# Kernel tuning notes

Measured on AMD Instinct MI355X. Metric: run time of the kernel, lower is better.

The kernel has to match this reference:

```python
import jax, jax.numpy as jnp
import numpy as np

DIM = 96
DIM_OUT = 192
HEADS = 2
Q_STRIDE = 4
WINDOW_SIZE = 16  # flattened mask-unit size AFTER q pooling
HEAD_DIM = DIM_OUT // HEADS


def setup_inputs() -> dict:
    key = jax.random.key(0)
    k1, k2, k3, k4, k5 = jax.random.split(key, 5)
    B, N = 64, 3136  # 56x56 tokens, 49 windows of 64 tokens
    x = jax.random.normal(k1, (B, N, DIM), dtype=jnp.float32)
    # nn.Linear params (PyTorch layout: [out, in])
    s_qkv = 1.0 / np.sqrt(DIM)
    w_qkv = jax.random.uniform(k2, (3 * DIM_OUT, DIM), jnp.float32, -s_qkv, s_qkv)
    b_qkv = jax.random.uniform(k3, (3 * DIM_OUT,), jnp.float32, -s_qkv, s_qkv)
    s_proj = 1.0 / np.sqrt(DIM_OUT)
    w_proj = jax.random.uniform(k4, (DIM_OUT, DIM_OUT), jnp.float32, -s_proj, s_proj)
    b_proj = jax.random.uniform(k5, (DIM_OUT,), jnp.float32, -s_proj, s_proj)
    return {"x": x, "w_qkv": w_qkv, "b_qkv": b_qkv, "w_proj": w_proj, "b_proj": b_proj}


def reference(x, w_qkv, b_qkv, w_proj, b_proj):
    B, N, _ = x.shape
    num_windows = N // (Q_STRIDE * WINDOW_SIZE)
    tokens_per_win = Q_STRIDE * WINDOW_SIZE  # 64
    # QKV projection; token axis splits as (tokens_per_win, num_windows)
    qkv = (x @ w_qkv.T + b_qkv).reshape(B, tokens_per_win, num_windows, 3, HEADS, HEAD_DIM)
    qkv = jnp.transpose(qkv, (3, 0, 4, 2, 1, 5))  # [3, B, H, W, T, D]
    q, k, v = qkv[0], qkv[1], qkv[2]
    # q pooling via strided amax over q_stride
    q = q.reshape(B, HEADS, num_windows, Q_STRIDE, WINDOW_SIZE, HEAD_DIM).max(axis=3)
    scale = HEAD_DIM ** (-0.5)
    attn = jax.nn.softmax(jnp.einsum('bhwqd,bhwkd->bhwqk', q * scale, k), axis=-1)
    o = jnp.einsum('bhwqk,bhwkd->bhwqd', attn, v)  # [B, H, W, WINDOW_SIZE, D]
    # transpose(1,3) then flatten -> [B, WINDOW_SIZE*num_windows, dim_out]
    o = jnp.transpose(o, (0, 3, 2, 1, 4)).reshape(B, -1, DIM_OUT)
    return o @ w_proj.T + b_proj
```

## Files before the change

### kernel.cpp

```cpp
#include <hip/hip_runtime.h>


#define NW 49
#define NTOK 3136
#define DIM 96
#define DOUT 192

#define WSQ 0
#define WSBQ 55296
#define WSP 55872
#define WSBP 92736
#define WSTOT 92928

typedef __bf16 bf16x8 __attribute__((ext_vector_type(8)));
typedef float f32x4 __attribute__((ext_vector_type(4)));
typedef unsigned short u16x8 __attribute__((ext_vector_type(8)));
typedef unsigned short u16x4 __attribute__((ext_vector_type(4)));

__device__ __forceinline__ unsigned short f2bf(float f) {
    unsigned int u = __builtin_bit_cast(unsigned int, f);
    u = (u + 0x7FFFu + ((u >> 16) & 1u)) >> 16;
    return (unsigned short)u;
}
__device__ __forceinline__ float bf2f(unsigned short h) {
    unsigned int u = ((unsigned int)h) << 16;
    return __builtin_bit_cast(float, u);
}

__device__ __forceinline__ bool sniff_fp32(const unsigned short* x16) {
    int sane = 0;
    #pragma unroll
    for (int i = 0; i < 32; ++i) {
        unsigned e = ((unsigned)x16[2 * i] >> 7) & 0xFFu;
        sane += (e >= 100u && e <= 141u) ? 1 : 0;
    }
    return sane < 24;
}

__device__ __forceinline__ bf16x8 ldb(const unsigned short* p) {
    return __builtin_bit_cast(bf16x8, *(const u16x8*)p);
}

__global__ __launch_bounds__(256)
void conv_weights(const void* __restrict__ x,
                  const void* __restrict__ w_qkv, const void* __restrict__ b_qkv,
                  const void* __restrict__ w_proj, const void* __restrict__ b_proj,
                  unsigned short* __restrict__ ws)
{
    const bool f32m = sniff_fp32((const unsigned short*)x);
    int t = blockIdx.x * 256 + threadIdx.x;
    if (t >= WSTOT / 8) return;
    int off = t * 8;
    const void* src;
    int rel;
    if (off < WSBQ)      { src = w_qkv;  rel = off; }
    else if (off < WSP)  { src = b_qkv;  rel = off - WSBQ; }
    else if (off < WSBP) { src = w_proj; rel = off - WSP; }
    else                 { src = b_proj; rel = off - WSBP; }
    u16x8 v;
    if (f32m) {
        const float* p = (const float*)src + rel;
        f32x4 a = *(const f32x4*)p;
        f32x4 bb = *(const f32x4*)(p + 4);
        v[0] = f2bf(a[0]);  v[1] = f2bf(a[1]);  v[2] = f2bf(a[2]);  v[3] = f2bf(a[3]);
        v[4] = f2bf(bb[0]); v[5] = f2bf(bb[1]); v[6] = f2bf(bb[2]); v[7] = f2bf(bb[3]);
    } else {
        v = *(const u16x8*)((const unsigned short*)src + rel);
    }
    *(u16x8*)(ws + off) = v;
}

__global__ __launch_bounds__(256, 2)
void mua_main(const void* __restrict__ x,
              const unsigned short* __restrict__ ws,
              void* __restrict__ out)
{
    const int bid = blockIdx.x;
    const int b   = bid / NW;
    const int wi  = bid - b * NW;
    const int tid  = threadIdx.x;
    const int wave = tid >> 6;
    const int lane = tid & 63;
    const int quad = lane >> 4;
    const int l16  = lane & 15;

    __shared__ __attribute__((aligned(16))) unsigned short lds[32768];
    unsigned short* k_s  = lds;
    unsigned short* v_s  = lds + 13312;
    unsigned short* qp_s = lds + 27136;
    unsigned short* p_s  = lds + 30464;
    unsigned short* x_s  = k_s;
    unsigned short* o_s  = qp_s;

    const int nbase = wave * 144;
    bf16x8 wfr[9][3];
    float  biasq[9];
    #pragma unroll
    for (int nt = 0; nt < 9; ++nt) {
        const int c = nbase + nt * 16 + l16;
        #pragma unroll
        for (int ks = 0; ks < 3; ++ks)
            wfr[nt][ks] = ldb(ws + WSQ + c * 96 + ks * 32 + quad * 8);
        biasq[nt] = bf2f(ws[WSBQ + c]);
    }

    const bool f32m = sniff_fp32((const unsigned short*)x);

    {
        const size_t xoff = ((size_t)b * NTOK + wi) * DIM;
        if (f32m) {
            #pragma unroll
            for (int i = 0; i < 3; ++i) {
                int chunk = tid + i * 256;
                int row = chunk / 12;
                int c16 = chunk - row * 12;
                const float* p = (const float*)x + xoff + (size_t)row * (NW * DIM) + c16 * 8;
                f32x4 a = *(const f32x4*)p;
                f32x4 bb = *(const f32x4*)(p + 4);
                u16x8 r;
                r[0] = f2bf(a[0]);  r[1] = f2bf(a[1]);  r[2] = f2bf(a[2]);  r[3] = f2bf(a[3]);
                r[4] = f2bf(bb[0]); r[5] = f2bf(bb[1]); r[6] = f2bf(bb[2]); r[7] = f2bf(bb[3]);
                *(u16x8*)&x_s[row * 104 + c16 * 8] = r;
            }
        } else {
            #pragma unroll
            for (int i = 0; i < 3; ++i) {
                int chunk = tid + i * 256;
                int row = chunk / 12;
                int c16 = chunk - row * 12;
                const unsigned short* p = (const unsigned short*)x + xoff + (size_t)row * (NW * DIM) + c16 * 8;
                *(u16x8*)&x_s[row * 104 + c16 * 8] = *(const u16x8*)p;
            }
        }
    }
    __syncthreads();

    bf16x8 afr[4][3];
    #pragma unroll
    for (int mt = 0; mt < 4; ++mt)
        #pragma unroll
        for (int ks = 0; ks < 3; ++ks)
            afr[mt][ks] = ldb(&x_s[(mt * 16 + l16) * 104 + ks * 32 + quad * 8]);
    __syncthreads();

    #pragma unroll
    for (int nt = 0; nt < 9; ++nt) {
        f32x4 acc[4];
        #pragma unroll
        for (int mt = 0; mt < 4; ++mt) {
            acc[mt] = (f32x4){0.f, 0.f, 0.f, 0.f};
            #pragma unroll
            for (int ks = 0; ks < 3; ++ks)
                acc[mt] = __builtin_amdgcn_mfma_f32_16x16x32_bf16(afr[mt][ks], wfr[nt][ks], acc[mt], 0, 0, 0);
        }
        const int c = nbase + nt * 16 + l16;
        const float bias = biasq[nt];
        const int type = c / 192;
        const int hd   = (c % 192) / 96;
        const int d    = c % 96;
        if (type == 0) {
            #pragma unroll
            for (int r = 0; r < 4; ++r) {
                float m = fmaxf(fmaxf(acc[0][r], acc[1][r]), fmaxf(acc[2][r], acc[3][r])) + bias;
                qp_s[(hd * 16 + quad * 4 + r) * 104 + d] = f2bf(m);
            }
        } else if (type == 1) {
            #pragma unroll
            for (int mt = 0; mt < 4; ++mt)
                #pragma unroll
                for (int r = 0; r < 4; ++r)
                    k_s[hd * 6656 + (mt * 16 + quad * 4 + r) * 104 + d] = f2bf(acc[mt][r] + bias);
        } else {
            #pragma unroll
            for (int mt = 0; mt < 4; ++mt) {
                u16x4 pk;
                #pragma unroll
                for (int r = 0; r < 4; ++r) pk[r] = f2bf(acc[mt][r] + bias);
                *(u16x4*)&v_s[hd * 6912 + d * 72 + mt * 16 + quad * 4] = pk;
            }
        }
    }

    const int cbase = wave * 48;
    bf16x8 wpr[3][6];
    float  biasp[3];
    #pragma unroll
    for (int i = 0; i < 3; ++i) {
        const int c = cbase + i * 16 + l16;
        #pragma unroll
        for (int ks = 0; ks < 6; ++ks)
            wpr[i][ks] = ldb(ws + WSP + c * 192 + ks * 32 + quad * 8);
        biasp[i] = bf2f(ws[WSBP + c]);
    }
    __syncthreads();

    const int h   = wave >> 1;
    const int sub = wave & 1;
    bf16x8 qa[3];
    #pragma unroll
    for (int ks = 0; ks < 3; ++ks)
        qa[ks] = ldb(&qp_s[(h * 16 + l16) * 104 + ks * 32 + quad * 8]);
    f32x4 s[4];
    #pragma unroll
    for (int nt = 0; nt < 4; ++nt) {
        s[nt] = (f32x4){0.f, 0.f, 0.f, 0.f};
        #pragma unroll
        for (int ks = 0; ks < 3; ++ks) {
            bf16x8 kb = ldb(&k_s[h * 6656 + (nt * 16 + l16) * 104 + ks * 32 + quad * 8]);
            s[nt] = __builtin_amdgcn_mfma_f32_16x16x32_bf16(qa[ks], kb, s[nt], 0, 0, 0);
        }
    }
    float rinv[4];
    const float cexp = 0.10206207261596576f * 1.4426950408889634f;
    #pragma unroll
    for (int r = 0; r < 4; ++r) {
        float m = fmaxf(fmaxf(s[0][r], s[1][r]), fmaxf(s[2][r], s[3][r]));
        m = fmaxf(m, __shfl_xor(m, 1));
        m = fmaxf(m, __shfl_xor(m, 2));
        m = fmaxf(m, __shfl_xor(m, 4));
        m = fmaxf(m, __shfl_xor(m, 8));
        float sum = 0.f;
        #pragma unroll
        for (int nt = 0; nt < 4; ++nt) {
            s[nt][r] = exp2f((s[nt][r] - m) * cexp);
            sum += s[nt][r];
        }
        sum += __shfl_xor(sum, 1);
        sum += __shfl_xor(sum, 2);
        sum += __shfl_xor(sum, 4);
        sum += __shfl_xor(sum, 8);
        rinv[r] = 1.0f / sum;
    }
    if (sub == 0) {
        #pragma unroll
        for (int nt = 0; nt < 4; ++nt)
            #pragma unroll
            for (int r = 0; r < 4; ++r)
                p_s[h * 1152 + (quad * 4 + r) * 72 + nt * 16 + l16] = f2bf(s[nt][r]);
    }
    __syncthreads();

    bf16x8 pa[2];
    #pragma unroll
    for (int ks = 0; ks < 2; ++ks)
        pa[ks] = ldb(&p_s[h * 1152 + l16 * 72 + ks * 32 + quad * 8]);
    #pragma unroll
    for (int i = 0; i < 3; ++i) {
        const int n0 = (sub * 3 + i) * 16;
        f32x4 oacc = (f32x4){0.f, 0.f, 0.f, 0.f};
        #pragma unroll
        for (int ks = 0; ks < 2; ++ks) {
            bf16x8 vb = ldb(&v_s[h * 6912 + (n0 + l16) * 72 + ks * 32 + quad * 8]);
            oacc = __builtin_amdgcn_mfma_f32_16x16x32_bf16(pa[ks], vb, oacc, 0, 0, 0);
        }
        #pragma unroll
        for (int r = 0; r < 4; ++r)
            o_s[(quad * 4 + r) * 200 + h * 96 + n0 + l16] = f2bf(oacc[r] * rinv[r]);
    }
    __syncthreads();

    bf16x8 oa[6];
    #pragma unroll
    for (int ks = 0; ks < 6; ++ks)
        oa[ks] = ldb(&o_s[l16 * 200 + ks * 32 + quad * 8]);
    #pragma unroll
    for (int i = 0; i < 3; ++i) {
        const int c = cbase + i * 16 + l16;
        f32x4 acc = (f32x4){0.f, 0.f, 0.f, 0.f};
        #pragma unroll
        for (int ks = 0; ks < 6; ++ks)
            acc = __builtin_amdgcn_mfma_f32_16x16x32_bf16(oa[ks], wpr[i][ks], acc, 0, 0, 0);
        const float bias = biasp[i];
        #pragma unroll
        for (int r = 0; r < 4; ++r) {
            const int m = quad * 4 + r;
            const size_t idx = ((size_t)(b * 784 + m * NW + wi)) * DOUT + c;
            if (f32m) ((float*)out)[idx] = acc[r] + bias;
            else      ((unsigned short*)out)[idx] = f2bf(acc[r] + bias);
        }
    }
}

extern "C" void kernel_launch(void* const* d_in, const int* in_sizes, int n_in,
                              void* d_out, int out_size, void* d_ws, size_t ws_size,
                              hipStream_t stream) {
    const void* x      = d_in[0];
    const void* w_qkv  = d_in[1];
    const void* b_qkv  = d_in[2];
    const void* w_proj = d_in[3];
    const void* b_proj = d_in[4];
    unsigned short* ws = (unsigned short*)d_ws;

    dim3 gridc((WSTOT / 8 + 255) / 256), blockc(256);
    hipLaunchKernelGGL(conv_weights, gridc, blockc, 0, stream,
                       x, w_qkv, b_qkv, w_proj, b_proj, ws);

    dim3 grid(64 * NW), block(256);
    hipLaunchKernelGGL(mua_main, grid, block, 0, stream, x, ws, d_out);
}
```

Baseline: 187.3 us.

## Split QKV projection into QK then V phases to shrink LDS and raise occupancy

```diff
diff --git a/kernel.cpp b/kernel.cpp
--- a/kernel.cpp
+++ b/kernel.cpp
@@ -18,9 +18,7 @@
 typedef unsigned short u16x4 __attribute__((ext_vector_type(4)));
 
 __device__ __forceinline__ unsigned short f2bf(float f) {
-    unsigned int u = __builtin_bit_cast(unsigned int, f);
-    u = (u + 0x7FFFu + ((u >> 16) & 1u)) >> 16;
-    return (unsigned short)u;
+    return __builtin_bit_cast(unsigned short, (__bf16)f);
 }
 __device__ __forceinline__ float bf2f(unsigned short h) {
     unsigned int u = ((unsigned int)h) << 16;
@@ -70,7 +68,7 @@
     *(u16x8*)(ws + off) = v;
 }
 
-__global__ __launch_bounds__(256, 2)
+__global__ __launch_bounds__(256, 4)
 void mua_main(const void* __restrict__ x,
               const unsigned short* __restrict__ ws,
               void* __restrict__ out)
@@ -84,23 +82,22 @@
     const int quad = lane >> 4;
     const int l16  = lane & 15;
 
-    __shared__ __attribute__((aligned(16))) unsigned short lds[32768];
+    __shared__ __attribute__((aligned(16))) unsigned short lds[19456];
+    unsigned short* x_s  = lds;
     unsigned short* k_s  = lds;
-    unsigned short* v_s  = lds + 13312;
-    unsigned short* qp_s = lds + 27136;
-    unsigned short* p_s  = lds + 30464;
-    unsigned short* x_s  = k_s;
-    unsigned short* o_s  = qp_s;
-
-    const int nbase = wave * 144;
-    bf16x8 wfr[9][3];
-    float  biasq[9];
-    #pragma unroll
-    for (int nt = 0; nt < 9; ++nt) {
-        const int c = nbase + nt * 16 + l16;
+    unsigned short* v_s  = lds;
+    unsigned short* qp_s = lds + 13824;
+    unsigned short* o_s  = lds + 13824;
+    unsigned short* p_s  = lds + 17152;
+
+    bf16x8 wq[6][3];
+    float  biasq[6];
+    #pragma unroll
+    for (int nt = 0; nt < 6; ++nt) {
+        const int c = (nt * 4 + wave) * 16 + l16;
         #pragma unroll
         for (int ks = 0; ks < 3; ++ks)
-            wfr[nt][ks] = ldb(ws + WSQ + c * 96 + ks * 32 + quad * 8);
+            wq[nt][ks] = ldb(ws + WSQ + c * 96 + ks * 32 + quad * 8);
         biasq[nt] = bf2f(ws[WSBQ + c]);
     }
 
@@ -144,53 +141,46 @@
     __syncthreads();
 
     #pragma unroll
-    for (int nt = 0; nt < 9; ++nt) {
+    for (int nt = 0; nt < 6; ++nt) {
         f32x4 acc[4];
         #pragma unroll
         for (int mt = 0; mt < 4; ++mt) {
             acc[mt] = (f32x4){0.f, 0.f, 0.f, 0.f};
             #pragma unroll
             for (int ks = 0; ks < 3; ++ks)
-                acc[mt] = __builtin_amdgcn_mfma_f32_16x16x32_bf16(afr[mt][ks], wfr[nt][ks], acc[mt], 0, 0, 0);
-        }
-        const int c = nbase + nt * 16 + l16;
+                acc[mt] = __builtin_amdgcn_mfma_f32_16x16x32_bf16(afr[mt][ks], wq[nt][ks], acc[mt], 0, 0, 0);
+        }
+        const int tt = nt * 4 + wave;
         const float bias = biasq[nt];
-        const int type = c / 192;
-        const int hd   = (c % 192) / 96;
-        const int d    = c % 96;
-        if (type == 0) {
+        if (nt < 3) {
+            const int hd = tt / 6;
+            const int d  = (tt % 6) * 16 + l16;
             #pragma unroll
             for (int r = 0; r < 4; ++r) {
                 float m = fmaxf(fmaxf(acc[0][r], acc[1][r]), fmaxf(acc[2][r], acc[3][r])) + bias;
                 qp_s[(hd * 16 + quad * 4 + r) * 104 + d] = f2bf(m);
             }
-        } else if (type == 1) {
+        } else {
+            const int tk = tt - 12;
+            const int hd = tk / 6;
+            const int d  = (tk % 6) * 16 + l16;
             #pragma unroll
             for (int mt = 0; mt < 4; ++mt)
                 #pragma unroll
                 for (int r = 0; r < 4; ++r)
                     k_s[hd * 6656 + (mt * 16 + quad * 4 + r) * 104 + d] = f2bf(acc[mt][r] + bias);
-        } else {
-            #pragma unroll
-            for (int mt = 0; mt < 4; ++mt) {
-                u16x4 pk;
-                #pragma unroll
-                for (int r = 0; r < 4; ++r) pk[r] = f2bf(acc[mt][r] + bias);
-                *(u16x4*)&v_s[hd * 6912 + d * 72 + mt * 16 + quad * 4] = pk;
-            }
-        }
-    }
-
-    const int cbase = wave * 48;
-    bf16x8 wpr[3][6];
-    float  biasp[3];
-    #pragma unroll
-    for (int i = 0; i < 3; ++i) {
-        const int c = cbase + i * 16 + l16;
-        #pragma unroll
-        for (int ks = 0; ks < 6; ++ks)
-            wpr[i][ks] = ldb(ws + WSP + c * 192 + ks * 32 + quad * 8);
-        biasp[i] = bf2f(ws[WSBP + c]);
+        }
+    }
+
+    bf16x8 wv[3][3];
+    float  biasv[3];
+    #pragma unroll
+    for (int i = 0; i < 3; ++i) {
+        const int c = 384 + (i * 4 + wave) * 16 + l16;
+        #pragma unroll
+        for (int ks = 0; ks < 3; ++ks)
+            wv[i][ks] = ldb(ws + WSQ + c * 96 + ks * 32 + quad * 8);
+        biasv[i] = bf2f(ws[WSBQ + c]);
     }
     __syncthreads();
 
@@ -237,6 +227,42 @@
             #pragma unroll
             for (int r = 0; r < 4; ++r)
                 p_s[h * 1152 + (quad * 4 + r) * 72 + nt * 16 + l16] = f2bf(s[nt][r]);
+    }
+    __syncthreads();
+
+    #pragma unroll
+    for (int i = 0; i < 3; ++i) {
+        f32x4 acc[4];
+        #pragma unroll
+        for (int mt = 0; mt < 4; ++mt) {
+            acc[mt] = (f32x4){0.f, 0.f, 0.f, 0.f};
+            #pragma unroll
+            for (int ks = 0; ks < 3; ++ks)
+                acc[mt] = __builtin_amdgcn_mfma_f32_16x16x32_bf16(afr[mt][ks], wv[i][ks], acc[mt], 0, 0, 0);
+        }
+        const int tv = i * 4 + wave;
+        const int hd = tv / 6;
+        const int d  = (tv % 6) * 16 + l16;
+        const float bias = biasv[i];
+        #pragma unroll
+        for (int mt = 0; mt < 4; ++mt) {
+            u16x4 pk;
+            #pragma unroll
+            for (int r = 0; r < 4; ++r) pk[r] = f2bf(acc[mt][r] + bias);
+            *(u16x4*)&v_s[hd * 6912 + d * 72 + mt * 16 + quad * 4] = pk;
+        }
+    }
+
+    const int cbase = wave * 48;
+    bf16x8 wpr[3][6];
+    float  biasp[3];
+    #pragma unroll
+    for (int i = 0; i < 3; ++i) {
+        const int c = cbase + i * 16 + l16;
+        #pragma unroll
+        for (int ks = 0; ks < 6; ++ks)
+            wpr[i][ks] = ldb(ws + WSP + c * 192 + ks * 32 + quad * 8);
+        biasp[i] = bf2f(ws[WSBP + c]);
     }
     __syncthreads();
 
```

New measurement: 201.3 us. 7.5% more time.
